# Kernel optimization log

Measured on AMD Instinct MI355X. Metric: run time of the kernel, lower is better.

## Reference

```python
import jax, jax.numpy as jnp
import numpy as np

NUM_EXPERTS = 16
TOP_K = 2
AUX_LOSS_COEF = 0.01


def setup_inputs() -> dict:
    key = jax.random.key(0)
    ks = jax.random.split(key, 5)
    B, S, D, I, E = 4, 2048, 1024, 2816, NUM_EXPERTS
    scale = 0.02
    return {
        "x": jax.random.normal(ks[0], (B, S, D), dtype=jnp.float32),
        "gate_w": jax.random.normal(ks[1], (D, E), dtype=jnp.float32) * scale,
        "Wg": jax.random.normal(ks[2], (E, D, I), dtype=jnp.float32) * scale,
        "Wu": jax.random.normal(ks[3], (E, D, I), dtype=jnp.float32) * scale,
        "Wd": jax.random.normal(ks[4], (E, I, D), dtype=jnp.float32) * scale,
    }


def _moe_forward(x, gate_w, Wg, Wu, Wd):
    B, S, D = x.shape
    E = gate_w.shape[1]
    # Router
    logits = x @ gate_w                      # [B,S,E]
    probs = jax.nn.softmax(logits, axis=-1)  # [B,S,E]
    topk_w, topk_idx = jax.lax.top_k(probs, TOP_K)        # [B,S,K]
    topk_w = topk_w / jnp.sum(topk_w, axis=-1, keepdims=True)
    # Per-token combine weight for each expert: [B,S,E]
    onehot = jax.nn.one_hot(topk_idx, E, dtype=x.dtype)   # [B,S,K,E]
    combine_w = jnp.einsum("bsk,bske->bse", topk_w, onehot)
    x_flat = x.reshape(-1, D)                # [T,D]
    w_flat = combine_w.reshape(-1, E)        # [T,E]
    # Accumulate weighted expert outputs (loop over fixed small E; unselected
    # tokens get zero weight, identical math to masked gather/scatter).
    out = jnp.zeros_like(x_flat)
    for e in range(E):
        h = jax.nn.silu(x_flat @ Wg[e]) * (x_flat @ Wu[e])  # [T,I]
        out = out + (h @ Wd[e]) * w_flat[:, e:e + 1]
    out = out.reshape(B, S, D)
    # Load balancing aux loss
    expert_mask = onehot.sum(axis=2)                        # [B,S,E]
    tokens_per_expert = expert_mask.mean(axis=(0, 1))       # [E]
    router_prob_per_expert = probs.mean(axis=(0, 1))        # [E]
    aux_loss = AUX_LOSS_COEF * jnp.sum(tokens_per_expert * router_prob_per_expert) * E
    return out, aux_loss


def reference(x, gate_w, Wg, Wu, Wd):
    return _moe_forward(x, gate_w, Wg, Wu, Wd)
```

## Files before the change

kernel.cpp:

```cpp
#include <hip/hip_runtime.h>
#include <stdint.h>

#define T_TOKENS 8192
#define D_DIM 1024
#define I_DIM 2816
#define E_NUM 16
#define N_SLOTS 16384

typedef float f32x4 __attribute__((ext_vector_type(4)));
typedef short s16x8 __attribute__((ext_vector_type(8)));
typedef short s16x4 __attribute__((ext_vector_type(4)));
typedef unsigned short u16;
typedef unsigned int u32;

__device__ __forceinline__ u16 f2bf(float f) {
  u32 u = __builtin_bit_cast(u32, f);
  u = (u + 0x7FFFu + ((u >> 16) & 1u)) >> 16;
  return (u16)u;
}
__device__ __forceinline__ u32 pack2(float a, float b) {
  return (u32)f2bf(a) | ((u32)f2bf(b) << 16);
}
__device__ __forceinline__ void async_load16(const void* g, void* l) {
  __builtin_amdgcn_global_load_lds(
      (const __attribute__((address_space(1))) void*)g,
      (__attribute__((address_space(3))) void*)l, 16, 0, 0);
}

__global__ void router_kernel(const float* __restrict__ x,
                              const float* __restrict__ gw,
                              int* __restrict__ e12, float* __restrict__ w12,
                              int* __restrict__ cnt, float* __restrict__ probsum) {
  __shared__ float sProb[E_NUM];
  __shared__ int sCnt[E_NUM];
  int tid = threadIdx.x;
  if (tid < E_NUM) { sProb[tid] = 0.f; sCnt[tid] = 0; }
  __syncthreads();
  int g = tid >> 4, i = tid & 15;
  int t = blockIdx.x * 16 + g;
  float acc[E_NUM];
#pragma unroll
  for (int e = 0; e < E_NUM; e++) acc[e] = 0.f;
  const f32x4* x4 = (const f32x4*)(x + (size_t)t * D_DIM);
  const f32x4* g4 = (const f32x4*)gw;
  for (int jj = 0; jj < 16; jj++) {
    f32x4 xv = x4[i + 16 * jj];
    int jb = 4 * (i + 16 * jj);
#pragma unroll
    for (int r = 0; r < 4; r++) {
      float xs = xv[r];
#pragma unroll
      for (int e4 = 0; e4 < 4; e4++) {
        f32x4 gv = g4[(jb + r) * 4 + e4];
        acc[e4 * 4 + 0] += xs * gv[0];
        acc[e4 * 4 + 1] += xs * gv[1];
        acc[e4 * 4 + 2] += xs * gv[2];
        acc[e4 * 4 + 3] += xs * gv[3];
      }
    }
  }
#pragma unroll
  for (int e = 0; e < E_NUM; e++) {
    float v = acc[e];
    v += __shfl_down(v, 8, 16);
    v += __shfl_down(v, 4, 16);
    v += __shfl_down(v, 2, 16);
    v += __shfl_down(v, 1, 16);
    acc[e] = v;
  }
  if (i == 0) {
    float mx = acc[0];
#pragma unroll
    for (int e = 1; e < E_NUM; e++) mx = fmaxf(mx, acc[e]);
    float p[E_NUM]; float s = 0.f;
#pragma unroll
    for (int e = 0; e < E_NUM; e++) { p[e] = __expf(acc[e] - mx); s += p[e]; }
    float inv = 1.f / s;
#pragma unroll
    for (int e = 0; e < E_NUM; e++) p[e] *= inv;
    int e1 = 0; float p1 = p[0];
#pragma unroll
    for (int e = 1; e < E_NUM; e++) if (p[e] > p1) { p1 = p[e]; e1 = e; }
    int e2 = (e1 == 0) ? 1 : 0; float p2 = p[e2];
#pragma unroll
    for (int e = 0; e < E_NUM; e++) if (e != e1 && p[e] > p2) { p2 = p[e]; e2 = e; }
    float wsum = p1 + p2;
    e12[2 * t] = e1; e12[2 * t + 1] = e2;
    w12[2 * t] = p1 / wsum; w12[2 * t + 1] = p2 / wsum;
#pragma unroll
    for (int e = 0; e < E_NUM; e++) atomicAdd(&sProb[e], p[e]);
    atomicAdd(&sCnt[e1], 1);
    atomicAdd(&sCnt[e2], 1);
  }
  __syncthreads();
  if (tid < E_NUM) {
    atomicAdd(&cnt[tid], sCnt[tid]);
    atomicAdd(&probsum[tid], sProb[tid]);
  }
}

__global__ void prefix_kernel(const int* __restrict__ cnt, int* __restrict__ offsets,
                              const float* __restrict__ probsum, float* __restrict__ aux_out) {
  if (threadIdx.x == 0) {
    int s = 0;
    for (int e = 0; e < E_NUM; e++) { offsets[e] = s; s += cnt[e]; }
    offsets[E_NUM] = s;
    float a = 0.f;
    for (int e = 0; e < E_NUM; e++) a += (float)cnt[e] * probsum[e];
    aux_out[0] = 0.01f * 16.f * a / (8192.f * 8192.f);
  }
}

__global__ void build_kernel(const int* __restrict__ e12, const float* __restrict__ w12,
                             const int* __restrict__ offsets, int* __restrict__ cursor,
                             int* __restrict__ tlist, float* __restrict__ wlist) {
  int t = blockIdx.x * 256 + threadIdx.x;
  if (t >= T_TOKENS) return;
#pragma unroll
  for (int k = 0; k < 2; k++) {
    int e = e12[2 * t + k];
    int pos = atomicAdd(&cursor[e], 1);
    int idx = offsets[e] + pos;
    tlist[idx] = t;
    wlist[idx] = w12[2 * t + k];
  }
}

__global__ void gather_kernel(const float* __restrict__ x, const int* __restrict__ tlist,
                              u16* __restrict__ Xe) {
  int r = blockIdx.x * 4 + (threadIdx.x >> 6);
  int lane = threadIdx.x & 63;
  int tok = tlist[r];
  const f32x4* src = (const f32x4*)(x + (size_t)tok * D_DIM);
  u32* dst = (u32*)(Xe + (size_t)r * D_DIM);
#pragma unroll
  for (int c = 0; c < 4; c++) {
    f32x4 v = src[lane + 64 * c];
    dst[(lane + 64 * c) * 2] = pack2(v[0], v[1]);
    dst[(lane + 64 * c) * 2 + 1] = pack2(v[2], v[3]);
  }
}

template <int K, int N>
__global__ __launch_bounds__(256) void transpose_kernel(const float* __restrict__ W,
                                                        u16* __restrict__ Wt) {
  __shared__ u16 tile[64][66];
  int e = blockIdx.z;
  int k0 = blockIdx.x * 64;
  int n0 = blockIdx.y * 64;
  const float* Win = W + (size_t)e * K * N;
  u16* Wout = Wt + (size_t)e * N * K;
  int t = threadIdx.x;
  int r = t >> 4;
  int c4 = (t & 15) * 4;
#pragma unroll
  for (int rep = 0; rep < 4; rep++) {
    int k = r + rep * 16;
    f32x4 v = *(const f32x4*)(Win + (size_t)(k0 + k) * N + n0 + c4);
    *(u32*)&tile[k][c4] = pack2(v[0], v[1]);
    *(u32*)&tile[k][c4 + 2] = pack2(v[2], v[3]);
  }
  __syncthreads();
#pragma unroll
  for (int rep = 0; rep < 4; rep++) {
    int n = r + rep * 16;
    int k4 = c4;
    s16x4 o;
    o[0] = tile[k4 + 0][n];
    o[1] = tile[k4 + 1][n];
    o[2] = tile[k4 + 2][n];
    o[3] = tile[k4 + 3][n];
    *(s16x4*)(Wout + (size_t)(n0 + n) * K + k0 + k4) = o;
  }
}

__global__ __launch_bounds__(256, 2) void gemm_gu_kernel(
    const u16* __restrict__ Abuf, const u16* __restrict__ Bg, const u16* __restrict__ Bu,
    u16* __restrict__ Hbuf,
    const int* __restrict__ cnt, const int* __restrict__ offsets) {
  int e = blockIdx.z;
  int Me = cnt[e];
  int m0 = blockIdx.y * 128;
  if (m0 >= Me) return;
  int n0 = blockIdx.x * 128;
  int rowBase = offsets[e];
  const u16* Bge = Bg + (size_t)e * I_DIM * D_DIM;
  const u16* Bue = Bu + (size_t)e * I_DIM * D_DIM;

  __shared__ u16 Ash[128 * 32];
  __shared__ u16 Bgsh[128 * 32];
  __shared__ u16 Bush[128 * 32];

  int tid = threadIdx.x;
  int lane = tid & 63;
  int wv = tid >> 6;
  int mq = wv & 1, nq = wv >> 1;
  int lrow = lane & 15, lq = lane >> 4;

  f32x4 accg[4][4], accu[4][4];
#pragma unroll
  for (int a = 0; a < 4; a++)
#pragma unroll
    for (int b = 0; b < 4; b++) { accg[a][b] = (f32x4)0.f; accu[a][b] = (f32x4)0.f; }

  for (int k0 = 0; k0 < D_DIM; k0 += 32) {
#pragma unroll
    for (int rep = 0; rep < 2; rep++) {
      int idx = tid + 256 * rep;
      int row = idx >> 2, q = idx & 3;
      int ldso = (wv * 64 + 256 * rep) * 8;
      int gr = m0 + row;
      gr = (gr < Me) ? gr : (Me - 1);
      async_load16(Abuf + (size_t)(rowBase + gr) * D_DIM + k0 + q * 8, &Ash[ldso]);
      async_load16(Bge + (size_t)(n0 + row) * D_DIM + k0 + q * 8, &Bgsh[ldso]);
      async_load16(Bue + (size_t)(n0 + row) * D_DIM + k0 + q * 8, &Bush[ldso]);
    }
    __syncthreads();
    s16x8 af[4], bg[4], bu[4];
#pragma unroll
    for (int fm = 0; fm < 4; fm++)
      af[fm] = *(const s16x8*)&Ash[(mq * 64 + fm * 16 + lrow) * 32 + lq * 8];
#pragma unroll
    for (int fn = 0; fn < 4; fn++) {
      bg[fn] = *(const s16x8*)&Bgsh[(nq * 64 + fn * 16 + lrow) * 32 + lq * 8];
      bu[fn] = *(const s16x8*)&Bush[(nq * 64 + fn * 16 + lrow) * 32 + lq * 8];
    }
#pragma unroll
    for (int fm = 0; fm < 4; fm++)
#pragma unroll
      for (int fn = 0; fn < 4; fn++) {
        accg[fm][fn] = __builtin_amdgcn_mfma_f32_16x16x32_bf16(af[fm], bg[fn], accg[fm][fn], 0, 0, 0);
        accu[fm][fn] = __builtin_amdgcn_mfma_f32_16x16x32_bf16(af[fm], bu[fn], accu[fm][fn], 0, 0, 0);
      }
    __syncthreads();
  }
#pragma unroll
  for (int fm = 0; fm < 4; fm++) {
#pragma unroll
    for (int i = 0; i < 4; i++) {
      int m = m0 + mq * 64 + fm * 16 + lq * 4 + i;
      if (m >= Me) continue;
      size_t arow = (size_t)(rowBase + m);
#pragma unroll
      for (int fn = 0; fn < 4; fn++) {
        int col = n0 + nq * 64 + fn * 16 + lrow;
        float g = accg[fm][fn][i];
        float u = accu[fm][fn][i];
        float h = (g / (1.f + __expf(-g))) * u;
        Hbuf[arow * I_DIM + col] = f2bf(h);
      }
    }
  }
}

__global__ __launch_bounds__(256) void gemm_down_kernel(
    const u16* __restrict__ Abuf, const u16* __restrict__ Bd, float* __restrict__ out,
    const int* __restrict__ cnt, const int* __restrict__ offsets,
    const int* __restrict__ tlist, const float* __restrict__ wlist) {
  int e = blockIdx.z;
  int Me = cnt[e];
  int m0 = blockIdx.y * 128;
  if (m0 >= Me) return;
  int n0 = blockIdx.x * 128;
  int rowBase = offsets[e];
  const u16* Bde = Bd + (size_t)e * D_DIM * I_DIM;

  __shared__ u16 Ash[128 * 32];
  __shared__ u16 Bsh[128 * 32];

  int tid = threadIdx.x;
  int lane = tid & 63;
  int wv = tid >> 6;
  int mq = wv & 1, nq = wv >> 1;
  int lrow = lane & 15, lq = lane >> 4;

  f32x4 acc[4][4];
#pragma unroll
  for (int a = 0; a < 4; a++)
#pragma unroll
    for (int b = 0; b < 4; b++) acc[a][b] = (f32x4)0.f;

  for (int k0 = 0; k0 < I_DIM; k0 += 32) {
#pragma unroll
    for (int rep = 0; rep < 2; rep++) {
      int idx = tid + 256 * rep;
      int row = idx >> 2, q = idx & 3;
      int ldso = (wv * 64 + 256 * rep) * 8;
      int gr = m0 + row;
      gr = (gr < Me) ? gr : (Me - 1);
      async_load16(Abuf + (size_t)(rowBase + gr) * I_DIM + k0 + q * 8, &Ash[ldso]);
      async_load16(Bde + (size_t)(n0 + row) * I_DIM + k0 + q * 8, &Bsh[ldso]);
    }
    __syncthreads();
    s16x8 af[4], bfr[4];
#pragma unroll
    for (int fm = 0; fm < 4; fm++)
      af[fm] = *(const s16x8*)&Ash[(mq * 64 + fm * 16 + lrow) * 32 + lq * 8];
#pragma unroll
    for (int fn = 0; fn < 4; fn++)
      bfr[fn] = *(const s16x8*)&Bsh[(nq * 64 + fn * 16 + lrow) * 32 + lq * 8];
#pragma unroll
    for (int fm = 0; fm < 4; fm++)
#pragma unroll
      for (int fn = 0; fn < 4; fn++)
        acc[fm][fn] = __builtin_amdgcn_mfma_f32_16x16x32_bf16(af[fm], bfr[fn], acc[fm][fn], 0, 0, 0);
    __syncthreads();
  }
#pragma unroll
  for (int fm = 0; fm < 4; fm++) {
#pragma unroll
    for (int i = 0; i < 4; i++) {
      int m = m0 + mq * 64 + fm * 16 + lq * 4 + i;
      if (m >= Me) continue;
      size_t arow = (size_t)(rowBase + m);
      int tok = tlist[arow];
      float w = wlist[arow];
#pragma unroll
      for (int fn = 0; fn < 4; fn++) {
        int col = n0 + nq * 64 + fn * 16 + lrow;
        atomicAdd(&out[(size_t)tok * D_DIM + col], acc[fm][fn][i] * w);
      }
    }
  }
}

extern "C" void kernel_launch(void* const* d_in, const int* in_sizes, int n_in,
                              void* d_out, int out_size, void* d_ws, size_t ws_size,
                              hipStream_t stream) {
  const float* x  = (const float*)d_in[0];
  const float* gw = (const float*)d_in[1];
  const float* Wg = (const float*)d_in[2];
  const float* Wu = (const float*)d_in[3];
  const float* Wd = (const float*)d_in[4];
  float* outf = (float*)d_out;
  char* ws = (char*)d_ws;
  int*   cnt     = (int*)(ws + 0);
  int*   cursor  = (int*)(ws + 64);
  float* probsum = (float*)(ws + 128);
  int*   offsets = (int*)(ws + 192);
  int*   e12     = (int*)(ws + 512);
  float* w12     = (float*)(ws + 66048);
  int*   tlist   = (int*)(ws + 131584);
  float* wlist   = (float*)(ws + 197120);
  u16*   Xe      = (u16*)(ws + (1 << 20));
  u16*   H       = (u16*)(ws + 34603008);
  u16*   WtA     = (u16*)(ws + 134217728);
  u16*   WtB     = (u16*)(ws + 234881024);

  hipMemsetAsync(d_out, 0, (size_t)(T_TOKENS * D_DIM + 1) * sizeof(float), stream);
  hipMemsetAsync(d_ws, 0, 512, stream);

  router_kernel<<<512, 256, 0, stream>>>(x, gw, e12, w12, cnt, probsum);
  prefix_kernel<<<1, 64, 0, stream>>>(cnt, offsets, probsum, outf + (size_t)(T_TOKENS * D_DIM));
  build_kernel<<<32, 256, 0, stream>>>(e12, w12, offsets, cursor, tlist, wlist);
  gather_kernel<<<4096, 256, 0, stream>>>(x, tlist, Xe);

  transpose_kernel<D_DIM, I_DIM><<<dim3(16, 44, E_NUM), 256, 0, stream>>>(Wg, WtA);
  transpose_kernel<D_DIM, I_DIM><<<dim3(16, 44, E_NUM), 256, 0, stream>>>(Wu, WtB);

  gemm_gu_kernel<<<dim3(22, 64, E_NUM), 256, 0, stream>>>(Xe, WtA, WtB, H, cnt, offsets);

  transpose_kernel<I_DIM, D_DIM><<<dim3(44, 16, E_NUM), 256, 0, stream>>>(Wd, WtA);

  gemm_down_kernel<<<dim3(8, 64, E_NUM), 256, 0, stream>>>(H, WtA, outf, cnt, offsets, tlist, wlist);
}
```

Before: 1.133 ms.

## Rework gate/up GEMM with double-buffered LDS, larger tiles and swizzle

Rewrites the fused gate/up expert GEMM to use 512-thread blocks with 256-row M tiles, a K step of 64, and double-buffered LDS staging driven by manual vmcnt waits. Global loads for the next stages now overlap MFMA work instead of waiting behind a full sync each step. An XOR swizzle on LDS rows reduces bank conflicts, and s_setprio raises priority around the MFMA bursts. In exchange it uses 128KB of LDS per block and adds extra barriers, which lowers occupancy, and larger M tiles waste more padded rows for experts with few tokens.

```diff
diff --git a/kernel.cpp b/kernel.cpp
--- a/kernel.cpp
+++ b/kernel.cpp
@@ -174,28 +174,31 @@
   }
 }
 
-__global__ __launch_bounds__(256, 2) void gemm_gu_kernel(
+__global__ __launch_bounds__(512, 2) void gemm_gu_kernel(
     const u16* __restrict__ Abuf, const u16* __restrict__ Bg, const u16* __restrict__ Bu,
     u16* __restrict__ Hbuf,
     const int* __restrict__ cnt, const int* __restrict__ offsets) {
   int e = blockIdx.z;
   int Me = cnt[e];
-  int m0 = blockIdx.y * 128;
+  int m0 = blockIdx.y * 256;
   if (m0 >= Me) return;
   int n0 = blockIdx.x * 128;
   int rowBase = offsets[e];
   const u16* Bge = Bg + (size_t)e * I_DIM * D_DIM;
   const u16* Bue = Bu + (size_t)e * I_DIM * D_DIM;
 
-  __shared__ u16 Ash[128 * 32];
-  __shared__ u16 Bgsh[128 * 32];
-  __shared__ u16 Bush[128 * 32];
+  __shared__ u16 lds[65536];
+  constexpr int A0 = 0, A1 = 16384;
+  constexpr int Bg0 = 32768, Bg1 = 40960;
+  constexpr int Bu0 = 49152, Bu1 = 57344;
 
   int tid = threadIdx.x;
   int lane = tid & 63;
   int wv = tid >> 6;
-  int mq = wv & 1, nq = wv >> 1;
+  int wm = wv >> 1;
+  int wn = wv & 1;
   int lrow = lane & 15, lq = lane >> 4;
+  int swz = lrow & 7;
 
   f32x4 accg[4][4], accu[4][4];
 #pragma unroll
@@ -203,47 +206,94 @@
 #pragma unroll
     for (int b = 0; b < 4; b++) { accg[a][b] = (f32x4)0.f; accu[a][b] = (f32x4)0.f; }
 
-  for (int k0 = 0; k0 < D_DIM; k0 += 32) {
-#pragma unroll
-    for (int rep = 0; rep < 2; rep++) {
-      int idx = tid + 256 * rep;
-      int row = idx >> 2, q = idx & 3;
-      int ldso = (wv * 64 + 256 * rep) * 8;
-      int gr = m0 + row;
-      gr = (gr < Me) ? gr : (Me - 1);
-      async_load16(Abuf + (size_t)(rowBase + gr) * D_DIM + k0 + q * 8, &Ash[ldso]);
-      async_load16(Bge + (size_t)(n0 + row) * D_DIM + k0 + q * 8, &Bgsh[ldso]);
-      async_load16(Bue + (size_t)(n0 + row) * D_DIM + k0 + q * 8, &Bush[ldso]);
-    }
-    __syncthreads();
-    s16x8 af[4], bg[4], bu[4];
-#pragma unroll
-    for (int fm = 0; fm < 4; fm++)
-      af[fm] = *(const s16x8*)&Ash[(mq * 64 + fm * 16 + lrow) * 32 + lq * 8];
-#pragma unroll
-    for (int fn = 0; fn < 4; fn++) {
-      bg[fn] = *(const s16x8*)&Bgsh[(nq * 64 + fn * 16 + lrow) * 32 + lq * 8];
-      bu[fn] = *(const s16x8*)&Bush[(nq * 64 + fn * 16 + lrow) * 32 + lq * 8];
-    }
-#pragma unroll
-    for (int fm = 0; fm < 4; fm++)
+  auto STAGE = [&](int kt, int b) {
+    int k0 = kt << 6;
+#pragma unroll
+    for (int r = 0; r < 4; r++) {
+      int c = tid + 512 * r;
+      int row = c >> 3, slot = c & 7;
+      int gr = m0 + row; gr = (gr < Me) ? gr : (Me - 1);
+      const u16* src = Abuf + (size_t)(rowBase + gr) * D_DIM + k0 + ((slot ^ (row & 7)) << 3);
+      async_load16(src, (void*)&lds[(b ? A1 : A0) + (wv * 64 + 512 * r) * 8]);
+    }
+#pragma unroll
+    for (int r = 0; r < 2; r++) {
+      int c = tid + 512 * r;
+      int row = c >> 3, slot = c & 7;
+      int col = k0 + ((slot ^ (row & 7)) << 3);
+      int ldso = (wv * 64 + 512 * r) * 8;
+      async_load16(Bge + (size_t)(n0 + row) * D_DIM + col, (void*)&lds[(b ? Bg1 : Bg0) + ldso]);
+      async_load16(Bue + (size_t)(n0 + row) * D_DIM + col, (void*)&lds[(b ? Bu1 : Bu0) + ldso]);
+    }
+  };
+
+  STAGE(0, 0);
+  STAGE(1, 1);
+
+  for (int kt = 0; kt < 16; kt++) {
+    int cur = kt & 1;
+    if (kt < 15) asm volatile("s_waitcnt vmcnt(8)");
+    else         asm volatile("s_waitcnt vmcnt(0)");
+    __builtin_amdgcn_s_barrier();
+    __builtin_amdgcn_sched_barrier(0);
+
+    const u16* As = lds + (cur ? A1 : A0);
+    const u16* Bgs = lds + (cur ? Bg1 : Bg0);
+    const u16* Bus = lds + (cur ? Bu1 : Bu0);
+
+#pragma unroll
+    for (int kh = 0; kh < 2; kh++) {
+      s16x8 af[4], bb[4];
+      int so = ((kh * 4 + lq) ^ swz) << 3;
+#pragma unroll
+      for (int fm = 0; fm < 4; fm++) {
+        int row = wm * 64 + fm * 16 + lrow;
+        af[fm] = *(const s16x8*)&As[row * 64 + so];
+      }
 #pragma unroll
       for (int fn = 0; fn < 4; fn++) {
-        accg[fm][fn] = __builtin_amdgcn_mfma_f32_16x16x32_bf16(af[fm], bg[fn], accg[fm][fn], 0, 0, 0);
-        accu[fm][fn] = __builtin_amdgcn_mfma_f32_16x16x32_bf16(af[fm], bu[fn], accu[fm][fn], 0, 0, 0);
-      }
-    __syncthreads();
-  }
+        int row = wn * 64 + fn * 16 + lrow;
+        bb[fn] = *(const s16x8*)&Bgs[row * 64 + so];
+      }
+      __builtin_amdgcn_s_barrier();
+      __builtin_amdgcn_s_setprio(1);
+#pragma unroll
+      for (int fm = 0; fm < 4; fm++)
+#pragma unroll
+        for (int fn = 0; fn < 4; fn++)
+          accg[fm][fn] = __builtin_amdgcn_mfma_f32_16x16x32_bf16(af[fm], bb[fn], accg[fm][fn], 0, 0, 0);
+      __builtin_amdgcn_s_setprio(0);
+      __builtin_amdgcn_s_barrier();
+#pragma unroll
+      for (int fn = 0; fn < 4; fn++) {
+        int row = wn * 64 + fn * 16 + lrow;
+        bb[fn] = *(const s16x8*)&Bus[row * 64 + so];
+      }
+      __builtin_amdgcn_s_barrier();
+      __builtin_amdgcn_s_setprio(1);
+#pragma unroll
+      for (int fm = 0; fm < 4; fm++)
+#pragma unroll
+        for (int fn = 0; fn < 4; fn++)
+          accu[fm][fn] = __builtin_amdgcn_mfma_f32_16x16x32_bf16(af[fm], bb[fn], accu[fm][fn], 0, 0, 0);
+      __builtin_amdgcn_s_setprio(0);
+      __builtin_amdgcn_s_barrier();
+    }
+
+    __builtin_amdgcn_sched_barrier(0);
+    if (kt + 2 < 16) STAGE(kt + 2, cur);
+  }
+
 #pragma unroll
   for (int fm = 0; fm < 4; fm++) {
 #pragma unroll
     for (int i = 0; i < 4; i++) {
-      int m = m0 + mq * 64 + fm * 16 + lq * 4 + i;
+      int m = m0 + wm * 64 + fm * 16 + lq * 4 + i;
       if (m >= Me) continue;
       size_t arow = (size_t)(rowBase + m);
 #pragma unroll
       for (int fn = 0; fn < 4; fn++) {
-        int col = n0 + nq * 64 + fn * 16 + lrow;
+        int col = n0 + wn * 64 + fn * 16 + lrow;
         float g = accg[fm][fn][i];
         float u = accu[fm][fn][i];
         float h = (g / (1.f + __expf(-g))) * u;
@@ -358,7 +408,7 @@
   transpose_kernel<D_DIM, I_DIM><<<dim3(16, 44, E_NUM), 256, 0, stream>>>(Wg, WtA);
   transpose_kernel<D_DIM, I_DIM><<<dim3(16, 44, E_NUM), 256, 0, stream>>>(Wu, WtB);
 
-  gemm_gu_kernel<<<dim3(22, 64, E_NUM), 256, 0, stream>>>(Xe, WtA, WtB, H, cnt, offsets);
+  gemm_gu_kernel<<<dim3(22, 32, E_NUM), 512, 0, stream>>>(Xe, WtA, WtB, H, cnt, offsets);
 
   transpose_kernel<I_DIM, D_DIM><<<dim3(44, 16, E_NUM), 256, 0, stream>>>(Wd, WtA);
 
```

New measurement: 1.135 ms. Within noise of the previous version (+0.2%).
